# Kernel tuning notes

Hardware: AMD Instinct MI355X
Metric: run time of the kernel (lower is better)

## Reference

```python
import jax, jax.numpy as jnp
import numpy as np

B, T, U = 8, 256, 64
ENC_DIM, DEC_DIM, JOINT_DIM, VOCAB = 512, 512, 640, 1024


def setup_inputs() -> dict:
    key = jax.random.key(0)
    k1, k2, k3, k4, k5 = jax.random.split(key, 5)
    s_enc = 1.0 / np.sqrt(ENC_DIM)
    s_dec = 1.0 / np.sqrt(DEC_DIM)
    s_joint = 1.0 / np.sqrt(JOINT_DIM)
    return {
        "enc_out": jax.random.normal(k1, (B, T, ENC_DIM), dtype=jnp.float32),
        "pred_out": jax.random.normal(k2, (B, U, DEC_DIM), dtype=jnp.float32),
        # nn.Linear weights stored as [out, in], applied as x @ W.T
        "W_enc": jax.random.uniform(k3, (JOINT_DIM, ENC_DIM), jnp.float32, -s_enc, s_enc),
        "W_pred": jax.random.uniform(k4, (JOINT_DIM, DEC_DIM), jnp.float32, -s_dec, s_dec),
        "W_out": jax.random.uniform(k5, (VOCAB, JOINT_DIM), jnp.float32, -s_joint, s_joint),
    }


def reference(enc_out, pred_out, W_enc, W_pred, W_out):
    # project: [B,T,J] and [B,U,J]
    enc_p = jnp.einsum("bte,je->btj", enc_out, W_enc)
    pred_p = jnp.einsum("bud,jd->buj", pred_out, W_pred)
    # broadcast add -> [B,T,U,J], SiLU, then output GEMM -> [B,T,U,V]
    joint = enc_p[:, :, None, :] + pred_p[:, None, :, :]
    joint = joint * jax.nn.sigmoid(joint)  # SiLU
    out = jnp.einsum("btuj,vj->btuv", joint, W_out)
    return out
```

## Files before the change

kernel.cpp:

```cpp
#include <hip/hip_runtime.h>

typedef unsigned short u16;
typedef __attribute__((ext_vector_type(8))) short short8;
typedef __attribute__((ext_vector_type(8))) unsigned short ushort8v;
typedef __attribute__((ext_vector_type(4))) float f32x4;

#define B_ 8
#define T_ 256
#define U_ 64
#define E_ 512
#define J_ 640
#define V_ 1024
#define NT 20

__device__ __forceinline__ u16 f2bf(float f) {
  unsigned int u = __float_as_uint(f);
  u += 0x7fffu + ((u >> 16) & 1u);
  return (u16)(u >> 16);
}

__device__ __forceinline__ void gload16(const void* g, void* l) {
  __builtin_amdgcn_global_load_lds((const __attribute__((address_space(1))) void*)g,
                                   (__attribute__((address_space(3))) void*)l,
                                   16, 0, 0);
}

__global__ __launch_bounds__(256) void cast5_k(const float4* __restrict__ s0,
                                               const float4* __restrict__ s1,
                                               const float4* __restrict__ s2,
                                               const float4* __restrict__ s3,
                                               const float4* __restrict__ s4,
                                               ushort4* __restrict__ dst) {
  int i = blockIdx.x * 256 + threadIdx.x;
  const int st = gridDim.x * 256;
  for (; i < 655360; i += st) {
    const float4* s; int off;
    if (i < 262144)      { s = s0; off = 0; }
    else if (i < 327680) { s = s1; off = 262144; }
    else if (i < 409600) { s = s2; off = 327680; }
    else if (i < 491520) { s = s3; off = 409600; }
    else                 { s = s4; off = 491520; }
    float4 v = s[i - off];
    ushort4 o;
    o.x = f2bf(v.x); o.y = f2bf(v.y); o.z = f2bf(v.z); o.w = f2bf(v.w);
    dst[i] = o;
  }
}

__global__ __launch_bounds__(256) void proj_k(const u16* __restrict__ X,
                                              const u16* __restrict__ W,
                                              float* __restrict__ C) {
  __shared__ __align__(16) u16 As[128 * 32];
  __shared__ __align__(16) u16 Bs[128 * 32];
  const int tid = threadIdx.x;
  const int w = tid >> 6, lane = tid & 63;
  const int wr = w >> 1, wc = w & 1;
  const int m0 = blockIdx.x * 128, n0 = blockIdx.y * 128;
  const int lr = lane & 15, lk = lane >> 4;
  const int r4 = tid >> 2, kq = tid & 3;

  f32x4 acc[4][4] = {};

  for (int ks = 0; ks < E_ / 32; ++ks) {
    const int k0 = ks * 32;
    gload16(X + (size_t)(m0 + r4) * E_ + k0 + kq * 8, (char*)As + w * 1024);
    gload16(X + (size_t)(m0 + 64 + r4) * E_ + k0 + kq * 8, (char*)As + 4096 + w * 1024);
    gload16(W + (size_t)(n0 + r4) * E_ + k0 + kq * 8, (char*)Bs + w * 1024);
    gload16(W + (size_t)(n0 + 64 + r4) * E_ + k0 + kq * 8, (char*)Bs + 4096 + w * 1024);
    __syncthreads();
    short8 a[4], bb[4];
#pragma unroll
    for (int m = 0; m < 4; ++m)
      a[m] = *(const short8*)&As[(wr * 64 + m * 16 + lr) * 32 + lk * 8];
#pragma unroll
    for (int n = 0; n < 4; ++n)
      bb[n] = *(const short8*)&Bs[(wc * 64 + n * 16 + lr) * 32 + lk * 8];
#pragma unroll
    for (int m = 0; m < 4; ++m)
#pragma unroll
      for (int n = 0; n < 4; ++n)
        acc[m][n] = __builtin_amdgcn_mfma_f32_16x16x32_bf16(a[m], bb[n], acc[m][n], 0, 0, 0);
    __syncthreads();
  }

#pragma unroll
  for (int m = 0; m < 4; ++m) {
    const int row = m0 + wr * 64 + m * 16 + lk * 4;
#pragma unroll
    for (int n = 0; n < 4; ++n) {
      const int col = n0 + wc * 64 + n * 16 + lr;
#pragma unroll
      for (int i = 0; i < 4; ++i)
        C[(size_t)(row + i) * J_ + col] = acc[m][n][i];
    }
  }
}

__global__ __launch_bounds__(256) void pack_k(const u16* __restrict__ Wo,
                                              u16* __restrict__ pk) {
  const int u = blockIdx.x * 256 + threadIdx.x;
  const int l = u & 63;
  int r = u >> 6;
  const int nq = r & 3;  r >>= 2;
  const int ks = r % 20;
  const int vt = r / 20;
  const int v = vt * 64 + nq * 16 + (l & 15);
  const int k = ks * 32 + (l >> 4) * 8;
  *(short8*)(pk + (size_t)u * 8) = *(const short8*)(Wo + (size_t)v * J_ + k);
}

__global__ __launch_bounds__(512, 2) void fused2_k(const float* __restrict__ ep,
                                                   const float* __restrict__ pp,
                                                   const u16* __restrict__ pk,
                                                   float* __restrict__ out) {
  __shared__ __align__(16) u16 Alds[64 * 640];
  const int tid = threadIdx.x;
  const int w = tid >> 6, lane = tid & 63;
  const int lr = lane & 15, lk = lane >> 4;
  const int bt = blockIdx.x;
  const int b = bt >> 8;
  const size_t m0 = (size_t)bt * 64;

  const float* eprow = ep + (size_t)bt * J_;
  const float* pbase = pp + (size_t)b * 64 * J_;
#pragma unroll
  for (int it = 0; it < 10; ++it) {
    const int unit = tid + it * 512;
    const int row = unit / 80;
    const int c = unit - row * 80;
    union { float4 v[2]; float f[8]; } Ee, Pp;
    Ee.v[0] = *(const float4*)(eprow + c * 8);
    Ee.v[1] = *(const float4*)(eprow + c * 8 + 4);
    Pp.v[0] = *(const float4*)(pbase + (size_t)row * J_ + c * 8);
    Pp.v[1] = *(const float4*)(pbase + (size_t)row * J_ + c * 8 + 4);
    union { ushort8v v; u16 s[8]; } R;
#pragma unroll
    for (int j = 0; j < 8; ++j) {
      float x = Ee.f[j] + Pp.f[j];
      R.s[j] = f2bf(x * __builtin_amdgcn_rcpf(1.0f + __expf(-x)));
    }
    *(ushort8v*)&Alds[row * 640 + ((c ^ (row & 7)) << 3)] = R.v;
  }
  __syncthreads();

  const int rx = lr & 7;
  int arow[4];
#pragma unroll
  for (int mq = 0; mq < 4; ++mq) arow[mq] = (mq * 16 + lr) * 640;

#define AR(aF, ks)                                                             \
  do {                                                                         \
    _Pragma("unroll")                                                          \
    for (int mq = 0; mq < 4; ++mq)                                             \
      aF[mq] = *(const short8*)&Alds[arow[mq] + ((((ks) * 4 + lk) ^ rx) << 3)];\
  } while (0)

#define BL(bF, ks)                                                             \
  do {                                                                         \
    _Pragma("unroll")                                                          \
    for (int nq = 0; nq < 4; ++nq)                                             \
      bF[nq] = *(const short8*)(bp + (ks) * 2048 + nq * 512);                  \
  } while (0)

#define MM(aF, bF)                                                             \
  do {                                                                         \
    __builtin_amdgcn_s_setprio(1);                                             \
    _Pragma("unroll")                                                          \
    for (int mq = 0; mq < 4; ++mq)                                             \
      _Pragma("unroll")                                                        \
      for (int nq = 0; nq < 4; ++nq)                                           \
        acc[mq][nq] = __builtin_amdgcn_mfma_f32_16x16x32_bf16(aF[mq], bF[nq],  \
                                                              acc[mq][nq], 0, 0, 0); \
    __builtin_amdgcn_s_setprio(0);                                             \
  } while (0)

#pragma unroll 1
  for (int c2 = 0; c2 < 2; ++c2) {
    const int vt = w * 2 + c2;
    const int col0 = vt * 64;
    const u16* bp = pk + (size_t)vt * 40960 + lane * 8;

    f32x4 acc[4][4] = {};
    short8 B0[4], B1[4], B2[4], B3[4], aE[4], aO[4];
    BL(B0, 0); BL(B1, 1);
    AR(aE, 0);
#pragma unroll 1
    for (int ks = 0; ks < NT; ks += 4) {
      BL(B2, ks + 2); AR(aO, ks + 1); MM(aE, B0);
      BL(B3, ks + 3); AR(aE, ks + 2); MM(aO, B1);
      if (ks + 4 < NT) BL(B0, ks + 4);
      AR(aO, ks + 3); MM(aE, B2);
      if (ks + 4 < NT) { BL(B1, ks + 5); AR(aE, ks + 4); }
      MM(aO, B3);
    }

#pragma unroll
    for (int mq = 0; mq < 4; ++mq) {
      const size_t row = m0 + mq * 16 + lk * 4;
#pragma unroll
      for (int nq = 0; nq < 4; ++nq) {
        const int col = col0 + nq * 16 + lr;
#pragma unroll
        for (int i = 0; i < 4; ++i)
          out[(row + i) * V_ + col] = acc[mq][nq][i];
      }
    }
  }
#undef AR
#undef BL
#undef MM
}

extern "C" void kernel_launch(void* const* d_in, const int* in_sizes, int n_in,
                              void* d_out, int out_size, void* d_ws, size_t ws_size,
                              hipStream_t stream) {
  const float* enc = (const float*)d_in[0];
  const float* pred = (const float*)d_in[1];
  const float* We = (const float*)d_in[2];
  const float* Wp = (const float*)d_in[3];
  const float* Wo = (const float*)d_in[4];
  float* out = (float*)d_out;

  char* ws = (char*)d_ws;
  u16* enc_bf = (u16*)ws;
  u16* pred_bf = (u16*)(ws + 2097152);
  u16* We_bf = (u16*)(ws + 2621440);
  u16* Wp_bf = (u16*)(ws + 3276800);
  u16* Wo_bf = (u16*)(ws + 3932160);
  float* ep = (float*)(ws + 5242880);
  float* pp = (float*)(ws + 10485760);
  u16* Wo_pk = (u16*)(ws + 11796480);

  cast5_k<<<2048, 256, 0, stream>>>((const float4*)enc, (const float4*)pred,
                                    (const float4*)We, (const float4*)Wp,
                                    (const float4*)Wo, (ushort4*)ws);

  proj_k<<<dim3(16, 5), 256, 0, stream>>>(enc_bf, We_bf, ep);
  proj_k<<<dim3(4, 5), 256, 0, stream>>>(pred_bf, Wp_bf, pp);
  pack_k<<<320, 256, 0, stream>>>(Wo_bf, Wo_pk);

  fused2_k<<<2048, 512, 0, stream>>>(ep, pp, Wo_pk, out);
}
```

Baseline: 238.2 us.

## Merge two column tiles per wave into one 64x128 pass with swapped MFMA operands

Each wave now computes both of its 64-column output tiles in a single K loop with a 4x8 accumulator, instead of two sequential passes. Each A fragment read from LDS is therefore reused across twice as many MFMAs, and LDS A reads are halved. The MFMA operands are swapped so each lane holds four consecutive columns, allowing float4 output stores in place of scalar stores. The first B fragment is prefetched before the SiLU/LDS fill and the pipeline is simplified to double buffering with sched barriers. The costs are higher register pressure (128 accumulator floats plus 16 B fragments) under launch_bounds(512,2), with a possible spill risk.

Result: slower. 250.8 us (+5.3%).

```diff
diff --git a/kernel.cpp b/kernel.cpp
--- a/kernel.cpp
+++ b/kernel.cpp
@@ -121,6 +121,22 @@
   const int b = bt >> 8;
   const size_t m0 = (size_t)bt * 64;
 
+  const u16* bp0 = pk + (size_t)(w * 2) * 40960 + lane * 8;
+  const u16* bp1 = bp0 + 40960;
+
+  short8 BE[8], BO[8], aE[4], aO[4];
+
+#define BL(bF, ks)                                                             \
+  do {                                                                         \
+    _Pragma("unroll")                                                          \
+    for (int nq = 0; nq < 4; ++nq) {                                           \
+      bF[nq]     = *(const short8*)(bp0 + (ks) * 2048 + nq * 512);             \
+      bF[4 + nq] = *(const short8*)(bp1 + (ks) * 2048 + nq * 512);             \
+    }                                                                          \
+  } while (0)
+
+  BL(BE, 0);
+
   const float* eprow = ep + (size_t)bt * J_;
   const float* pbase = pp + (size_t)b * 64 * J_;
 #pragma unroll
@@ -155,55 +171,40 @@
       aF[mq] = *(const short8*)&Alds[arow[mq] + ((((ks) * 4 + lk) ^ rx) << 3)];\
   } while (0)
 
-#define BL(bF, ks)                                                             \
-  do {                                                                         \
-    _Pragma("unroll")                                                          \
-    for (int nq = 0; nq < 4; ++nq)                                             \
-      bF[nq] = *(const short8*)(bp + (ks) * 2048 + nq * 512);                  \
-  } while (0)
-
 #define MM(aF, bF)                                                             \
   do {                                                                         \
     __builtin_amdgcn_s_setprio(1);                                             \
     _Pragma("unroll")                                                          \
     for (int mq = 0; mq < 4; ++mq)                                             \
       _Pragma("unroll")                                                        \
-      for (int nq = 0; nq < 4; ++nq)                                           \
-        acc[mq][nq] = __builtin_amdgcn_mfma_f32_16x16x32_bf16(aF[mq], bF[nq],  \
+      for (int nq = 0; nq < 8; ++nq)                                           \
+        acc[mq][nq] = __builtin_amdgcn_mfma_f32_16x16x32_bf16(bF[nq], aF[mq],  \
                                                               acc[mq][nq], 0, 0, 0); \
     __builtin_amdgcn_s_setprio(0);                                             \
   } while (0)
 
+  f32x4 acc[4][8] = {};
+  AR(aE, 0);
+
 #pragma unroll 1
-  for (int c2 = 0; c2 < 2; ++c2) {
-    const int vt = w * 2 + c2;
-    const int col0 = vt * 64;
-    const u16* bp = pk + (size_t)vt * 40960 + lane * 8;
-
-    f32x4 acc[4][4] = {};
-    short8 B0[4], B1[4], B2[4], B3[4], aE[4], aO[4];
-    BL(B0, 0); BL(B1, 1);
-    AR(aE, 0);
-#pragma unroll 1
-    for (int ks = 0; ks < NT; ks += 4) {
-      BL(B2, ks + 2); AR(aO, ks + 1); MM(aE, B0);
-      BL(B3, ks + 3); AR(aE, ks + 2); MM(aO, B1);
-      if (ks + 4 < NT) BL(B0, ks + 4);
-      AR(aO, ks + 3); MM(aE, B2);
-      if (ks + 4 < NT) { BL(B1, ks + 5); AR(aE, ks + 4); }
-      MM(aO, B3);
-    }
-
-#pragma unroll
-    for (int mq = 0; mq < 4; ++mq) {
-      const size_t row = m0 + mq * 16 + lk * 4;
-#pragma unroll
-      for (int nq = 0; nq < 4; ++nq) {
-        const int col = col0 + nq * 16 + lr;
-#pragma unroll
-        for (int i = 0; i < 4; ++i)
-          out[(row + i) * V_ + col] = acc[mq][nq][i];
-      }
+  for (int ks = 0; ks < NT; ks += 2) {
+    BL(BO, ks + 1);
+    AR(aO, ks + 1);
+    MM(aE, BE);
+    __builtin_amdgcn_sched_barrier(0);
+    if (ks + 2 < NT) { BL(BE, ks + 2); AR(aE, ks + 2); }
+    MM(aO, BO);
+    __builtin_amdgcn_sched_barrier(0);
+  }
+
+  const int col0 = w * 128;
+#pragma unroll
+  for (int mq = 0; mq < 4; ++mq) {
+    const size_t row = m0 + mq * 16 + lr;
+#pragma unroll
+    for (int nq = 0; nq < 8; ++nq) {
+      const int col = col0 + nq * 16 + lk * 4;
+      *(float4*)&out[row * V_ + col] = *(float4*)&acc[mq][nq];
     }
   }
 #undef AR
```
